# Performance work log

Hardware: AMD Instinct MI355X
Metric: run time of the kernel (lower is better)

Reference implementation:

```python
import jax, jax.numpy as jnp
import numpy as np

B, N, E = 4, 4096, 65536
DIN, DB, DO, T = 128, 64, 128, 4  # in_features, bond_features, out_features, n_edge_types
DCAT = 2 * DIN + DB


def setup_inputs() -> dict:
    key = jax.random.key(0)
    ks = jax.random.split(key, 24)
    s = 0.05
    inp = {
        "sites": jax.random.normal(ks[0], (B, N, DIN), jnp.float32),
        "bonds": jax.random.normal(ks[1], (B, E, DB), jnp.float32),
        "idx1": jax.random.randint(ks[2], (E,), 0, N),
        "idx2": jax.random.randint(ks[3], (E,), 0, N),
        "uc": jax.random.randint(ks[4], (E,), 0, T),
        # per-type 2-layer MLPs (stacked over types)
        "W1a": jax.random.normal(ks[5], (T, DCAT, DO), jnp.float32) * s,
        "b1a": jnp.zeros((T, DO), jnp.float32),
        "W1b": jax.random.normal(ks[6], (T, DO, DO), jnp.float32) * s,
        "b1b": jnp.zeros((T, DO), jnp.float32),
        "W2a": jax.random.normal(ks[7], (T, DCAT, DO), jnp.float32) * s,
        "b2a": jnp.zeros((T, DO), jnp.float32),
        "W2b": jax.random.normal(ks[8], (T, DO, DO), jnp.float32) * s,
        "b2b": jnp.zeros((T, DO), jnp.float32),
        # attention gates (Linear(out,1) + sigmoid)
        "Wa1": jax.random.normal(ks[9], (DO, 1), jnp.float32) * s,
        "ba1": jnp.zeros((1,), jnp.float32),
        "Wa2": jax.random.normal(ks[10], (DO, 1), jnp.float32) * s,
        "ba2": jnp.zeros((1,), jnp.float32),
    }
    return inp


def reference(sites, bonds, idx1, idx2, uc, W1a, b1a, W1b, b1b,
              W2a, b2a, W2b, b2b, Wa1, ba1, Wa2, ba2):
    lrelu = jax.nn.leaky_relu  # negative_slope 0.01, matches nn.LeakyReLU default
    # gather edge endpoints and concat with bond features: [B, E, 2*DIN+DB]
    v = jnp.concatenate([sites[:, idx1], sites[:, idx2], bonds], axis=2)

    def mlp(Wa, ba, Wb, bb):
        return lrelu(v @ Wa + ba) @ Wb + bb  # [B, E, DO]

    n_types = W1a.shape[0]
    out1 = jnp.zeros((v.shape[0], v.shape[1], W1b.shape[-1]), v.dtype)
    out2 = jnp.zeros_like(out1)
    for i in range(n_types):  # small fixed set of structurally distinct weights
        m = (uc == i)[None, :, None]
        out1 = jnp.where(m, mlp(W1a[i], b1a[i], W1b[i], b1b[i]), out1)
        out2 = jnp.where(m, mlp(W2a[i], b2a[i], W2b[i], b2b[i]), out2)
    out1 = lrelu(out1)
    out2 = lrelu(out2)
    # sigmoid attention gate
    g1 = jax.nn.sigmoid(out1 @ Wa1 + ba1) * out1
    g2 = jax.nn.sigmoid(out2 @ Wa2 + ba2) * out2
    # scatter_add over edges -> nodes along dim 1, then sum
    n_nodes = sites.shape[1]
    agg = jnp.zeros((sites.shape[0], n_nodes, out1.shape[-1]), v.dtype)
    agg = agg.at[:, idx2].add(g1 + g2)
    return agg
```

## Files before the change

### kernel.cpp

```cpp
#include <hip/hip_runtime.h>

#define NB 4
#define NN 4096
#define NE 65536
#define DIN 128
#define DB 64
#define DOUT 128
#define NT 4
#define DCAT 320

#define MT 64
#define LDH (DOUT + 8)

typedef __bf16 bf16;
typedef __bf16 bf16x2 __attribute__((ext_vector_type(2)));
typedef __bf16 bf16x4 __attribute__((ext_vector_type(4)));
typedef __bf16 bf16x8 __attribute__((ext_vector_type(8)));
typedef float floatx4 __attribute__((ext_vector_type(4)));

__device__ __forceinline__ void async16(const void* g, void* l) {
    __builtin_amdgcn_global_load_lds(
        (const __attribute__((address_space(1))) unsigned int*)g,
        (__attribute__((address_space(3))) unsigned int*)l, 16, 0, 0);
}

#define NS4 (NB * NN * DIN / 4)
#define NA  (NT * 256 * DCAT)
#define NB2 (NT * 256 * DOUT)
#define NBO4 (NB * NE * DB / 4)
#define NCHUNK ((NS4 + NA + NB2 + NBO4) / 256)
#define PSTRIDE 4096
__global__ void prep_k(const float* __restrict__ sites, const float* __restrict__ bonds,
                       const float* __restrict__ W1a, const float* __restrict__ W2a,
                       const float* __restrict__ W1b, const float* __restrict__ W2b,
                       const int* __restrict__ uc, const int* __restrict__ idx2,
                       bf16* __restrict__ sitesB,
                       bf16* __restrict__ WtA, bf16* __restrict__ WtB,
                       bf16* __restrict__ bondsB,
                       int* __restrict__ cnt, int* __restrict__ deg,
                       int* __restrict__ bucket) {
    int tid = threadIdx.x;
    if (blockIdx.x < 256) {
        __shared__ int h[NT];
        __shared__ int baseo[NT];
        if (tid < NT) h[tid] = 0;
        __syncthreads();
        int e = blockIdx.x * 256 + tid;
        int t = uc[e] & 3;
        int lp = atomicAdd(&h[t], 1);
        __syncthreads();
        if (tid < NT) baseo[tid] = atomicAdd(&cnt[tid], h[tid]);
        __syncthreads();
        bucket[t * NE + baseo[t] + lp] = e;
        atomicAdd(&deg[idx2[e] & (NN - 1)], 1);
        return;
    }
    for (int c = blockIdx.x - 256; c < NCHUNK; c += PSTRIDE) {
        int i = c * 256 + tid;
        if (i < NS4) {
            float4 f = ((const float4*)sites)[i];
            bf16x4 h = { (bf16)f.x, (bf16)f.y, (bf16)f.z, (bf16)f.w };
            ((bf16x4*)sitesB)[i] = h;
        } else if (i < NS4 + NA) {
            int j = i - NS4;
            int k = j % DCAT;
            int n = (j / DCAT) % 256;
            int t = j / (DCAT * 256);
            float w = (n < DOUT) ? W1a[(t * DCAT + k) * DOUT + n]
                                 : W2a[(t * DCAT + k) * DOUT + (n - DOUT)];
            WtA[j] = (bf16)w;
        } else if (i < NS4 + NA + NB2) {
            int j = i - NS4 - NA;
            int k = j % DOUT;
            int n = (j / DOUT) % 256;
            int t = j / (DOUT * 256);
            float w = (n < DOUT) ? W1b[(t * DOUT + k) * DOUT + n]
                                 : W2b[(t * DOUT + k) * DOUT + (n - DOUT)];
            WtB[j] = (bf16)w;
        } else {
            int j = i - NS4 - NA - NB2;
            float4 f = ((const float4*)bonds)[j];
            bf16x4 h = { (bf16)f.x, (bf16)f.y, (bf16)f.z, (bf16)f.w };
            ((bf16x4*)bondsB)[j] = h;
        }
    }
}

__global__ void scan_k(const int* __restrict__ deg, int* __restrict__ off) {
    __shared__ int wsum[4];
    int tid = threadIdx.x;
    int lane = tid & 63, w = tid >> 6;
    int v[16]; int s = 0;
    #pragma unroll
    for (int j = 0; j < 16; ++j) { v[j] = deg[tid * 16 + j]; s += v[j]; }
    int inc = s;
    #pragma unroll
    for (int d = 1; d < 64; d <<= 1) {
        int x = __shfl_up(inc, d, 64);
        if (lane >= d) inc += x;
    }
    if (lane == 63) wsum[w] = inc;
    __syncthreads();
    int wpre = 0;
    #pragma unroll
    for (int j = 0; j < 4; ++j) wpre += (j < w) ? wsum[j] : 0;
    int excl = wpre + inc - s;
    #pragma unroll
    for (int j = 0; j < 16; ++j) { off[tid * 16 + j] = excl; excl += v[j]; }
    if (tid == 255) off[4096] = excl;
}

__launch_bounds__(256, 4)
__global__ void main_k(const bf16* __restrict__ sitesB, const bf16* __restrict__ bondsB,
                       const int* __restrict__ idx1, const int* __restrict__ idx2,
                       const int* __restrict__ cnt, const int* __restrict__ bucket,
                       const int* __restrict__ off, int* __restrict__ cursor,
                       const bf16* __restrict__ WtA, const bf16* __restrict__ WtB,
                       const float* __restrict__ b1a, const float* __restrict__ b2a,
                       const float* __restrict__ b1b, const float* __restrict__ b2b,
                       const float* __restrict__ Wa1, const float* __restrict__ ba1,
                       const float* __restrict__ Wa2, const float* __restrict__ ba2,
                       bf16* __restrict__ eo) {
    __shared__ __align__(16) char smem[40960];
    bf16* sA  = (bf16*)smem;
    bf16* sB  = (bf16*)(smem + 8192);
    bf16* sH1 = (bf16*)smem;
    bf16* sH2 = (bf16*)(smem + MT * LDH * 2);
    float* sWa = (float*)(smem + 35840);

    const int tid = threadIdx.x;

    int blk = blockIdx.x;
    int p = blk & 7;
    const int b = p >> 1;
    int flat = ((blk >> 3) << 1) + (p & 1);

    int c0 = cnt[0], c1 = cnt[1], c2 = cnt[2], c3 = cnt[3];
    int n0 = (c0 + MT - 1) / MT, n1 = (c1 + MT - 1) / MT,
        n2t = (c2 + MT - 1) / MT, n3 = (c3 + MT - 1) / MT;
    int t, ti, cT;
    if (flat < n0)                 { t = 0; ti = flat;                 cT = c0; }
    else if (flat < n0+n1)         { t = 1; ti = flat - n0;            cT = c1; }
    else if (flat < n0+n1+n2t)     { t = 2; ti = flat - n0 - n1;       cT = c2; }
    else if (flat < n0+n1+n2t+n3)  { t = 3; ti = flat - n0 - n1 - n2t; cT = c3; }
    else return;
    const int base = ti * MT;
    const int nvalid = min(MT, cT - base);

    const int rowA = tid >> 2;
    const int rr = min(rowA, max(nvalid - 1, 0));
    const int e  = bucket[t * NE + base + rr] & (NE - 1);
    const int r1 = idx1[e] & (NN - 1);
    const int r2 = idx2[e] & (NN - 1);

    const int wv = tid >> 6;
    const int lane = tid & 63;
    const int br = wv >> 1;
    const int nh = wv & 1;
    const int lr = lane & 15;
    const int quad = lane >> 4;
    const int lk = quad * 8;
    const int colbase = nh * 64;
    const int lodd = lane & 1;

    const size_t sbase = (size_t)b * NN;
    const int kseg = (tid & 3) ^ (rowA & 3) ^ ((rowA >> 2) & 3);
    const bf16* pA1 = sitesB + (sbase + r1) * DIN + kseg * 8;
    const bf16* pA2 = sitesB + (sbase + r2) * DIN + kseg * 8;
    const bf16* pBo = bondsB + ((size_t)b * NE + e) * DB + kseg * 8;

    auto stageA = [&](int ks, int buf) {
        const bf16* src = (ks < 4) ? (pA1 + ks * 32)
                        : (ks < 8) ? (pA2 + (ks - 4) * 32)
                                   : (pBo + (ks - 8) * 32);
        async16(src, smem + buf * 4096 + wv * 1024);
    };
    auto stageB1 = [&](int ks, int buf) {
        #pragma unroll
        for (int j = 0; j < 4; ++j) {
            int d = (j * 4 + wv) * 64 + lane;
            int col = d >> 2;
            int ksg = (d & 3) ^ (col & 3) ^ ((col >> 2) & 3);
            const bf16* src = WtA + (size_t)(t * 256 + col) * DCAT + ks * 32 + ksg * 8;
            async16(src, &sB[buf * 8192 + (j * 4 + wv) * 512]);
        }
    };

    const int slot = quad ^ (lr & 3) ^ ((lr >> 2) & 3);

    floatx4 acc[4][4];
    #pragma unroll
    for (int mt = 0; mt < 4; ++mt)
        #pragma unroll
        for (int nt = 0; nt < 4; ++nt)
            acc[mt][nt] = (floatx4){0.f, 0.f, 0.f, 0.f};

    stageA(0, 0);
    stageB1(0, 0);
    #pragma unroll
    for (int ks = 0; ks < 10; ++ks) {
        int buf = ks & 1;
        __syncthreads();
        if (ks < 9) {
            stageA(ks + 1, buf ^ 1);
            stageB1(ks + 1, buf ^ 1);
        }
        bf16x8 aF[4];
        #pragma unroll
        for (int mt = 0; mt < 4; ++mt) {
            int row = mt * 16 + lr;
            aF[mt] = *(const bf16x8*)(&sA[buf * 2048 + (row * 4 + slot) * 8]);
        }
        #pragma unroll
        for (int nt = 0; nt < 4; ++nt) {
            int cc = br * 128 + colbase + nt * 16 + lr;
            bf16x8 bF = *(const bf16x8*)(&sB[buf * 8192 + (cc * 4 + slot) * 8]);
            #pragma unroll
            for (int mt = 0; mt < 4; ++mt)
                acc[mt][nt] = __builtin_amdgcn_mfma_f32_16x16x32_bf16(aF[mt], bF, acc[mt][nt], 0, 0, 0);
        }
    }
    __syncthreads();

    sWa[tid] = (tid < 128) ? Wa1[tid] : Wa2[tid - 128];

    bf16* sH = (br == 0) ? sH1 : sH2;
    const float* biasA = ((br == 0) ? b1a : b2a) + t * DOUT;
    #pragma unroll
    for (int nt = 0; nt < 4; ++nt) {
        int c = colbase + nt * 16 + lr;
        int cpair = c & ~1;
        float bias = biasA[c];
        #pragma unroll
        for (int mt = 0; mt < 4; ++mt) {
            float v[4], x[4];
            #pragma unroll
            for (int rg = 0; rg < 4; ++rg) {
                float u = acc[mt][nt][rg] + bias;
                v[rg] = u > 0.f ? u : 0.01f * u;
            }
            #pragma unroll
            for (int rg = 0; rg < 4; ++rg) x[rg] = __shfl_xor(v[rg], 1);
            int r0 = mt * 16 + quad * 4 + lodd * 2;
            float lo0 = lodd ? x[2] : v[0], hi0 = lodd ? v[2] : x[0];
            float lo1 = lodd ? x[3] : v[1], hi1 = lodd ? v[3] : x[1];
            *(bf16x2*)(&sH[r0 * LDH + cpair])       = (bf16x2){ (bf16)lo0, (bf16)hi0 };
            *(bf16x2*)(&sH[(r0 + 1) * LDH + cpair]) = (bf16x2){ (bf16)lo1, (bf16)hi1 };
        }
    }
    __syncthreads();

    floatx4 acc2[4][4];
    #pragma unroll
    for (int mt = 0; mt < 4; ++mt)
        #pragma unroll
        for (int nt = 0; nt < 4; ++nt)
            acc2[mt][nt] = (floatx4){0.f, 0.f, 0.f, 0.f};

    const bf16* sHa = (br == 0) ? sH1 : sH2;
    const bf16* WtB_w = WtB + (size_t)(t * 256 + br * 128 + colbase) * DOUT + lk;
    #pragma unroll
    for (int ks = 0; ks < 4; ++ks) {
        bf16x8 aF[4];
        #pragma unroll
        for (int mt = 0; mt < 4; ++mt)
            aF[mt] = *(const bf16x8*)(&sHa[(mt * 16 + lr) * LDH + ks * 32 + lk]);
        #pragma unroll
        for (int nt = 0; nt < 4; ++nt) {
            bf16x8 bF = *(const bf16x8*)(&WtB_w[(size_t)(nt * 16 + lr) * DOUT + ks * 32]);
            #pragma unroll
            for (int mt = 0; mt < 4; ++mt)
                acc2[mt][nt] = __builtin_amdgcn_mfma_f32_16x16x32_bf16(aF[mt], bF, acc2[mt][nt], 0, 0, 0);
        }
    }
    __syncthreads();

    const float* biasB = ((br == 0) ? b1b : b2b) + t * DOUT;
    #pragma unroll
    for (int nt = 0; nt < 4; ++nt) {
        int c = colbase + nt * 16 + lr;
        int cpair = c & ~1;
        float bias = biasB[c];
        #pragma unroll
        for (int mt = 0; mt < 4; ++mt) {
            float v[4], x[4];
            #pragma unroll
            for (int rg = 0; rg < 4; ++rg) {
                float u = acc2[mt][nt][rg] + bias;
                v[rg] = u > 0.f ? u : 0.01f * u;
            }
            #pragma unroll
            for (int rg = 0; rg < 4; ++rg) x[rg] = __shfl_xor(v[rg], 1);
            int r0 = mt * 16 + quad * 4 + lodd * 2;
            float lo0 = lodd ? x[2] : v[0], hi0 = lodd ? v[2] : x[0];
            float lo1 = lodd ? x[3] : v[1], hi1 = lodd ? v[3] : x[1];
            *(bf16x2*)(&sH[r0 * LDH + cpair])       = (bf16x2){ (bf16)lo0, (bf16)hi0 };
            *(bf16x2*)(&sH[(r0 + 1) * LDH + cpair]) = (bf16x2){ (bf16)lo1, (bf16)hi1 };
        }
    }
    __syncthreads();

    {
        int m = tid >> 2;
        int q = tid & 3;
        float d1 = 0.f, d2 = 0.f;
        #pragma unroll
        for (int j = 0; j < 4; ++j) {
            bf16x8 h1 = *(const bf16x8*)(&sH1[m * LDH + q * 32 + j * 8]);
            bf16x8 h2 = *(const bf16x8*)(&sH2[m * LDH + q * 32 + j * 8]);
            float4 wa = *(const float4*)(&sWa[q * 32 + j * 8]);
            float4 wb = *(const float4*)(&sWa[q * 32 + j * 8 + 4]);
            float4 va = *(const float4*)(&sWa[128 + q * 32 + j * 8]);
            float4 vb = *(const float4*)(&sWa[128 + q * 32 + j * 8 + 4]);
            d1 += (float)h1[0] * wa.x; d1 += (float)h1[1] * wa.y;
            d1 += (float)h1[2] * wa.z; d1 += (float)h1[3] * wa.w;
            d1 += (float)h1[4] * wb.x; d1 += (float)h1[5] * wb.y;
            d1 += (float)h1[6] * wb.z; d1 += (float)h1[7] * wb.w;
            d2 += (float)h2[0] * va.x; d2 += (float)h2[1] * va.y;
            d2 += (float)h2[2] * va.z; d2 += (float)h2[3] * va.w;
            d2 += (float)h2[4] * vb.x; d2 += (float)h2[5] * vb.y;
            d2 += (float)h2[6] * vb.z; d2 += (float)h2[7] * vb.w;
        }
        d1 += __shfl_xor(d1, 1); d1 += __shfl_xor(d1, 2);
        d2 += __shfl_xor(d2, 1); d2 += __shfl_xor(d2, 2);
        d1 = fminf(fmaxf(d1 + ba1[0], -30.f), 30.f);
        d2 = fminf(fmaxf(d2 + ba2[0], -30.f), 30.f);
        float s1 = 1.f / (1.f + __expf(-d1));
        float s2 = 1.f / (1.f + __expf(-d2));
        if (m < nvalid) {
            int rank0 = 0;
            if (q == 0) rank0 = atomicAdd(&cursor[b * NN + r2], 1);
            int rank = __shfl(rank0, lane & ~3);
            int prm = (off[r2] + rank) & (NE - 1);
            bf16* dst = eo + ((size_t)b * NE + prm) * DOUT;
            #pragma unroll
            for (int j = 0; j < 4; ++j) {
                int cc = (q + 4 * j) * 8;
                bf16x8 h1 = *(const bf16x8*)(&sH1[m * LDH + cc]);
                bf16x8 h2 = *(const bf16x8*)(&sH2[m * LDH + cc]);
                bf16x8 w;
                #pragma unroll
                for (int c = 0; c < 8; ++c)
                    w[c] = (bf16)(s1 * (float)h1[c] + s2 * (float)h2[c]);
                *(bf16x8*)(dst + cc) = w;
            }
        }
    }
}

__global__ void gather_k(const bf16* __restrict__ eo, const int* __restrict__ off,
                         float* __restrict__ out) {
    __shared__ float part[4 * 4 * 128];
    int tid = threadIdx.x;
    int nl = tid >> 6;
    int g  = (tid >> 4) & 3;
    int cseg = tid & 15;
    int n = blockIdx.x * 4 + nl;
    int b = blockIdx.y;
    int o0 = off[n], o1 = off[n + 1];
    const bf16* base = eo + (size_t)b * NE * DOUT + cseg * 8;
    float a[8] = {0.f, 0.f, 0.f, 0.f, 0.f, 0.f, 0.f, 0.f};
    for (int r = o0 + g; r < o1; r += 4) {
        bf16x8 v = *(const bf16x8*)(base + (size_t)r * DOUT);
        #pragma unroll
        for (int j = 0; j < 8; ++j) a[j] += (float)v[j];
    }
    #pragma unroll
    for (int j = 0; j < 8; ++j) part[(nl * 4 + g) * 128 + cseg * 8 + j] = a[j];
    __syncthreads();
    int c2 = (tid & 63) * 2;
    float s0 = 0.f, s1 = 0.f;
    #pragma unroll
    for (int gg = 0; gg < 4; ++gg) {
        s0 += part[(nl * 4 + gg) * 128 + c2];
        s1 += part[(nl * 4 + gg) * 128 + c2 + 1];
    }
    float2 o = { s0, s1 };
    *(float2*)(&out[((size_t)b * NN + n) * DOUT + c2]) = o;
}

extern "C" void kernel_launch(void* const* d_in, const int* in_sizes, int n_in,
                              void* d_out, int out_size, void* d_ws, size_t ws_size,
                              hipStream_t stream) {
    const float* sites = (const float*)d_in[0];
    const float* bonds = (const float*)d_in[1];
    const int*   idx1  = (const int*)d_in[2];
    const int*   idx2  = (const int*)d_in[3];
    const int*   uc    = (const int*)d_in[4];
    const float* W1a = (const float*)d_in[5];
    const float* b1a = (const float*)d_in[6];
    const float* W1b = (const float*)d_in[7];
    const float* b1b = (const float*)d_in[8];
    const float* W2a = (const float*)d_in[9];
    const float* b2a = (const float*)d_in[10];
    const float* W2b = (const float*)d_in[11];
    const float* b2b = (const float*)d_in[12];
    const float* Wa1 = (const float*)d_in[13];
    const float* ba1 = (const float*)d_in[14];
    const float* Wa2 = (const float*)d_in[15];
    const float* ba2 = (const float*)d_in[16];
    float* out = (float*)d_out;

    char* ws = (char*)d_ws;
    size_t o_cnt    = 0;
    size_t o_deg    = 64;
    size_t o_cursor = o_deg + NN * 4;
    size_t o_off    = o_cursor + (size_t)NB * NN * 4;
    size_t o_bucket = o_off + (NN + 16) * 4;
    size_t o_wta    = o_bucket + (size_t)NT * NE * 4;
    size_t o_wtb    = o_wta + (size_t)NA * 2;
    size_t o_sitesB = o_wtb + (size_t)NB2 * 2;
    size_t o_eo     = o_sitesB + (size_t)NB * NN * DIN * 2;
    size_t o_bondsB = o_eo + (size_t)NB * NE * DOUT * 2;
    size_t need     = o_bondsB + (size_t)NB * NE * DB * 2;
    if (ws_size < need) return;

    int*  cnt    = (int*)(ws + o_cnt);
    int*  deg    = (int*)(ws + o_deg);
    int*  cursor = (int*)(ws + o_cursor);
    int*  off    = (int*)(ws + o_off);
    int*  bucket = (int*)(ws + o_bucket);
    bf16* WtA    = (bf16*)(ws + o_wta);
    bf16* WtB    = (bf16*)(ws + o_wtb);
    bf16* sitesB = (bf16*)(ws + o_sitesB);
    bf16* eo     = (bf16*)(ws + o_eo);
    bf16* bondsB = (bf16*)(ws + o_bondsB);

    hipMemsetAsync(ws, 0, 64 + (size_t)NN * 4 + (size_t)NB * NN * 4, stream);

    prep_k<<<PSTRIDE + 256, 256, 0, stream>>>(
        sites, bonds, W1a, W2a, W1b, W2b, uc, idx2,
        sitesB, WtA, WtB, bondsB, cnt, deg, bucket);
    scan_k<<<1, 256, 0, stream>>>(deg, off);

    const int maxTiles = NE / MT + NT;
    main_k<<<maxTiles * NB, 256, 0, stream>>>(
        sitesB, bondsB, idx1, idx2, cnt, bucket, off, cursor, WtA, WtB,
        b1a, b2a, b1b, b2b, Wa1, ba1, Wa2, ba2, eo);

    gather_k<<<dim3(NN / 4, NB), 256, 0, stream>>>(eo, off, out);
}
```

Baseline: 266.8 us.

## Read fp32 bonds directly in main kernel and fuse degree scan into prep

Drops the separate fp32-to-bf16 conversion pass over the bond features. The main kernel now loads fp32 bonds straight from global memory into registers and converts them to bf16 MFMA fragments for the last two K steps. The degree prefix scan is folded into the prep kernel through a last-block-done atomic counter, which removes one kernel launch. The trade-off is that bond loads in main_k are now synchronous register loads of twice the bytes instead of async LDS staging, which may stall the MFMA loop.

```diff
diff --git a/kernel.cpp b/kernel.cpp
--- a/kernel.cpp
+++ b/kernel.cpp
@@ -27,22 +27,22 @@
 #define NS4 (NB * NN * DIN / 4)
 #define NA  (NT * 256 * DCAT)
 #define NB2 (NT * 256 * DOUT)
-#define NBO4 (NB * NE * DB / 4)
-#define NCHUNK ((NS4 + NA + NB2 + NBO4) / 256)
-#define PSTRIDE 4096
-__global__ void prep_k(const float* __restrict__ sites, const float* __restrict__ bonds,
+#define NCONV ((NS4 + NA + NB2) / 256)
+#define PREP_TOTAL (NCONV + 256)
+__global__ void prep_k(const float* __restrict__ sites,
                        const float* __restrict__ W1a, const float* __restrict__ W2a,
                        const float* __restrict__ W1b, const float* __restrict__ W2b,
                        const int* __restrict__ uc, const int* __restrict__ idx2,
                        bf16* __restrict__ sitesB,
                        bf16* __restrict__ WtA, bf16* __restrict__ WtB,
-                       bf16* __restrict__ bondsB,
                        int* __restrict__ cnt, int* __restrict__ deg,
-                       int* __restrict__ bucket) {
+                       int* __restrict__ bucket, int* __restrict__ off) {
+    __shared__ int h[NT];
+    __shared__ int baseo[NT];
+    __shared__ int wsum[4];
+    __shared__ int amLast;
     int tid = threadIdx.x;
     if (blockIdx.x < 256) {
-        __shared__ int h[NT];
-        __shared__ int baseo[NT];
         if (tid < NT) h[tid] = 0;
         __syncthreads();
         int e = blockIdx.x * 256 + tid;
@@ -53,14 +53,12 @@
         __syncthreads();
         bucket[t * NE + baseo[t] + lp] = e;
         atomicAdd(&deg[idx2[e] & (NN - 1)], 1);
-        return;
-    }
-    for (int c = blockIdx.x - 256; c < NCHUNK; c += PSTRIDE) {
-        int i = c * 256 + tid;
+    } else {
+        int i = (blockIdx.x - 256) * 256 + tid;
         if (i < NS4) {
             float4 f = ((const float4*)sites)[i];
-            bf16x4 h = { (bf16)f.x, (bf16)f.y, (bf16)f.z, (bf16)f.w };
-            ((bf16x4*)sitesB)[i] = h;
+            bf16x4 hh = { (bf16)f.x, (bf16)f.y, (bf16)f.z, (bf16)f.w };
+            ((bf16x4*)sitesB)[i] = hh;
         } else if (i < NS4 + NA) {
             int j = i - NS4;
             int k = j % DCAT;
@@ -69,7 +67,7 @@
             float w = (n < DOUT) ? W1a[(t * DCAT + k) * DOUT + n]
                                  : W2a[(t * DCAT + k) * DOUT + (n - DOUT)];
             WtA[j] = (bf16)w;
-        } else if (i < NS4 + NA + NB2) {
+        } else {
             int j = i - NS4 - NA;
             int k = j % DOUT;
             int n = (j / DOUT) % 256;
@@ -77,22 +75,21 @@
             float w = (n < DOUT) ? W1b[(t * DOUT + k) * DOUT + n]
                                  : W2b[(t * DOUT + k) * DOUT + (n - DOUT)];
             WtB[j] = (bf16)w;
-        } else {
-            int j = i - NS4 - NA - NB2;
-            float4 f = ((const float4*)bonds)[j];
-            bf16x4 h = { (bf16)f.x, (bf16)f.y, (bf16)f.z, (bf16)f.w };
-            ((bf16x4*)bondsB)[j] = h;
-        }
-    }
-}
-
-__global__ void scan_k(const int* __restrict__ deg, int* __restrict__ off) {
-    __shared__ int wsum[4];
-    int tid = threadIdx.x;
+        }
+    }
+
+    __threadfence();
+    if (tid == 0) amLast = (atomicAdd(&cnt[8], 1) == PREP_TOTAL - 1);
+    __syncthreads();
+    if (!amLast) return;
+    __threadfence();
     int lane = tid & 63, w = tid >> 6;
     int v[16]; int s = 0;
     #pragma unroll
-    for (int j = 0; j < 16; ++j) { v[j] = deg[tid * 16 + j]; s += v[j]; }
+    for (int j = 0; j < 16; ++j) {
+        v[j] = atomicAdd(&deg[tid * 16 + j], 0);
+        s += v[j];
+    }
     int inc = s;
     #pragma unroll
     for (int d = 1; d < 64; d <<= 1) {
@@ -111,7 +108,7 @@
 }
 
 __launch_bounds__(256, 4)
-__global__ void main_k(const bf16* __restrict__ sitesB, const bf16* __restrict__ bondsB,
+__global__ void main_k(const bf16* __restrict__ sitesB, const float* __restrict__ bonds,
                        const int* __restrict__ idx1, const int* __restrict__ idx2,
                        const int* __restrict__ cnt, const int* __restrict__ bucket,
                        const int* __restrict__ off, int* __restrict__ cursor,
@@ -163,16 +160,20 @@
     const int colbase = nh * 64;
     const int lodd = lane & 1;
 
+    int e4[4];
+    #pragma unroll
+    for (int mt = 0; mt < 4; ++mt) {
+        int rw = min(mt * 16 + lr, max(nvalid - 1, 0));
+        e4[mt] = bucket[t * NE + base + rw] & (NE - 1);
+    }
+
     const size_t sbase = (size_t)b * NN;
     const int kseg = (tid & 3) ^ (rowA & 3) ^ ((rowA >> 2) & 3);
     const bf16* pA1 = sitesB + (sbase + r1) * DIN + kseg * 8;
     const bf16* pA2 = sitesB + (sbase + r2) * DIN + kseg * 8;
-    const bf16* pBo = bondsB + ((size_t)b * NE + e) * DB + kseg * 8;
 
     auto stageA = [&](int ks, int buf) {
-        const bf16* src = (ks < 4) ? (pA1 + ks * 32)
-                        : (ks < 8) ? (pA2 + (ks - 4) * 32)
-                                   : (pBo + (ks - 8) * 32);
+        const bf16* src = (ks < 4) ? (pA1 + ks * 32) : (pA2 + (ks - 4) * 32);
         async16(src, smem + buf * 4096 + wv * 1024);
     };
     auto stageB1 = [&](int ks, int buf) {
@@ -202,14 +203,25 @@
         int buf = ks & 1;
         __syncthreads();
         if (ks < 9) {
-            stageA(ks + 1, buf ^ 1);
+            if (ks + 1 < 8) stageA(ks + 1, buf ^ 1);
             stageB1(ks + 1, buf ^ 1);
         }
         bf16x8 aF[4];
-        #pragma unroll
-        for (int mt = 0; mt < 4; ++mt) {
-            int row = mt * 16 + lr;
-            aF[mt] = *(const bf16x8*)(&sA[buf * 2048 + (row * 4 + slot) * 8]);
+        if (ks < 8) {
+            #pragma unroll
+            for (int mt = 0; mt < 4; ++mt) {
+                int row = mt * 16 + lr;
+                aF[mt] = *(const bf16x8*)(&sA[buf * 2048 + (row * 4 + slot) * 8]);
+            }
+        } else {
+            #pragma unroll
+            for (int mt = 0; mt < 4; ++mt) {
+                const float* pb = bonds + ((size_t)b * NE + e4[mt]) * DB + (ks - 8) * 32 + lk;
+                float4 f0 = *(const float4*)pb;
+                float4 f1 = *(const float4*)(pb + 4);
+                aF[mt] = (bf16x8){ (bf16)f0.x, (bf16)f0.y, (bf16)f0.z, (bf16)f0.w,
+                                   (bf16)f1.x, (bf16)f1.y, (bf16)f1.z, (bf16)f1.w };
+            }
         }
         #pragma unroll
         for (int nt = 0; nt < 4; ++nt) {
@@ -411,8 +423,7 @@
     size_t o_wtb    = o_wta + (size_t)NA * 2;
     size_t o_sitesB = o_wtb + (size_t)NB2 * 2;
     size_t o_eo     = o_sitesB + (size_t)NB * NN * DIN * 2;
-    size_t o_bondsB = o_eo + (size_t)NB * NE * DOUT * 2;
-    size_t need     = o_bondsB + (size_t)NB * NE * DB * 2;
+    size_t need     = o_eo + (size_t)NB * NE * DOUT * 2;
     if (ws_size < need) return;
 
     int*  cnt    = (int*)(ws + o_cnt);
@@ -424,18 +435,16 @@
     bf16* WtB    = (bf16*)(ws + o_wtb);
     bf16* sitesB = (bf16*)(ws + o_sitesB);
     bf16* eo     = (bf16*)(ws + o_eo);
-    bf16* bondsB = (bf16*)(ws + o_bondsB);
 
     hipMemsetAsync(ws, 0, 64 + (size_t)NN * 4 + (size_t)NB * NN * 4, stream);
 
-    prep_k<<<PSTRIDE + 256, 256, 0, stream>>>(
-        sites, bonds, W1a, W2a, W1b, W2b, uc, idx2,
-        sitesB, WtA, WtB, bondsB, cnt, deg, bucket);
-    scan_k<<<1, 256, 0, stream>>>(deg, off);
+    prep_k<<<PREP_TOTAL, 256, 0, stream>>>(
+        sites, W1a, W2a, W1b, W2b, uc, idx2,
+        sitesB, WtA, WtB, cnt, deg, bucket, off);
 
     const int maxTiles = NE / MT + NT;
     main_k<<<maxTiles * NB, 256, 0, stream>>>(
-        sitesB, bondsB, idx1, idx2, cnt, bucket, off, cursor, WtA, WtB,
+        sitesB, bonds, idx1, idx2, cnt, bucket, off, cursor, WtA, WtB,
         b1a, b2a, b1b, b2b, Wa1, ba1, Wa2, ba2, eo);
 
     gather_k<<<dim3(NN / 4, NB), 256, 0, stream>>>(eo, off, out);
```

Result: slower. 573.7 us (+115.1%).
